# Kernel optimization log

Hardware: AMD Instinct MI355X
Metric: run time of the kernel (lower is better)

Reference implementation:

```python
import jax, jax.numpy as jnp
import numpy as np

TOTAL = 16777216  # total nodes across all graphs
N = 65536         # number of graphs (len(v_count))
K = 16            # k_pool


def setup_inputs() -> dict:
    key = jax.random.key(0)
    k1, k2 = jax.random.split(key)
    Y = jax.random.normal(k1, (TOTAL, 1), dtype=jnp.float32)
    W = jnp.ones((K,), dtype=jnp.float32)  # initializer Ones, as in build()
    e_map = jnp.sort(jax.random.randint(k2, (TOTAL,), 0, N, dtype=jnp.int32))
    v_count = jnp.ones((N,), dtype=jnp.int32)  # only its length is used
    return {"Y": Y, "W": W, "e_map": e_map, "v_count": v_count}


def reference(Y, W, e_map, v_count):
    # Faithful SortPooling forward. Instead of materializing the padded
    # [N, max_seg_len] -inf tensor, we do k_pool fused segment-max passes:
    # each pass extracts the current per-segment max and masks out exactly
    # one occurrence (the first, by index) -- identical to tf.math.top_k on
    # the -inf-padded ragged-to-dense tensor (ties yield duplicate values,
    # matching top_k semantics).
    n = v_count.shape[0]
    k = W.shape[0]  # static k_pool; segments here are much larger than k
    y = jnp.squeeze(Y, axis=-1)  # [TOTAL]
    total = y.shape[0]
    idxs = jnp.arange(total, dtype=jnp.int32)
    neg_inf = jnp.float32(-jnp.inf)

    y_work = y
    tops = []
    for _ in range(k):
        m = jax.ops.segment_max(y_work, e_map, num_segments=n)  # [N]
        tops.append(m)
        is_max = y_work == m[e_map]
        # first index attaining the max in each segment (total == sentinel)
        first = jax.ops.segment_min(jnp.where(is_max, idxs, total),
                                    e_map, num_segments=n)  # [N]
        # OOB indices (exhausted/empty segments) are dropped by scatter
        y_work = y_work.at[first].set(neg_inf)

    Y_top = jnp.stack(tops, axis=-1)        # [N, k] sorted descending
    Wn = jax.nn.softmax(W)                  # [k]
    Y_w = jnp.where(jnp.isinf(Y_top), jnp.float32(0.0), Y_top) * Wn
    return jnp.sum(Y_w, axis=-1)            # [N]
```

## Files before the change

### kernel.cpp

```cpp
#include <hip/hip_runtime.h>
#include <math.h>

#define KPOOL 16
#define SPLIT 8

typedef float f32x4 __attribute__((ext_vector_type(4)));

__device__ __forceinline__ void ce(float& x, float& y) {
  float hi = fmaxf(x, y), lo = fminf(x, y);
  x = hi;
  y = lo;
}

__device__ __forceinline__ void sort8(float (&v)[8]) {
  ce(v[0], v[1]); ce(v[2], v[3]); ce(v[4], v[5]); ce(v[6], v[7]);
  ce(v[0], v[2]); ce(v[1], v[3]); ce(v[4], v[6]); ce(v[5], v[7]);
  ce(v[1], v[2]); ce(v[5], v[6]);
  ce(v[0], v[4]); ce(v[1], v[5]); ce(v[2], v[6]); ce(v[3], v[7]);
  ce(v[2], v[4]); ce(v[3], v[5]);
  ce(v[1], v[2]); ce(v[3], v[4]); ce(v[5], v[6]);
}

__device__ __forceinline__ void merge8into16(float (&t)[KPOOL], const float (&b)[8]) {
#pragma unroll
  for (int i = 8; i < 16; ++i) t[i] = fmaxf(t[i], b[15 - i]);
#pragma unroll
  for (int s = 8; s >= 1; s >>= 1) {
#pragma unroll
    for (int i = 0; i < 16; ++i)
      if ((i & s) == 0) ce(t[i], t[i + s]);
  }
}

__device__ __forceinline__ void merge_partner(float (&t)[KPOOL], int dist) {
  float c[KPOOL];
#pragma unroll
  for (int i = 0; i < KPOOL; ++i) {
    float o = __shfl_xor(t[KPOOL - 1 - i], dist);
    c[i] = fmaxf(t[i], o);
  }
#pragma unroll
  for (int s = 8; s >= 1; s >>= 1) {
#pragma unroll
    for (int i = 0; i < KPOOL; ++i)
      if ((i & s) == 0) ce(c[i], c[i + s]);
  }
#pragma unroll
  for (int i = 0; i < KPOOL; ++i) t[i] = c[i];
}

__device__ __forceinline__ int lower_bound_range(const int* __restrict__ a,
                                                 int lo, int hi, int key) {
  while (lo < hi) {
    int mid = (lo + hi) >> 1;
    if (a[mid] < key) lo = mid + 1;
    else hi = mid;
  }
  return lo;
}

__global__ __launch_bounds__(256)
void boundary_kernel(const int* __restrict__ emap, int total, int n,
                     int* __restrict__ starts, float* __restrict__ wn_out,
                     const float* __restrict__ W) {
  int g = blockIdx.x * 256 + threadIdx.x;
  if (g == 0) {
    float w[KPOOL], m = -INFINITY, s = 0.0f;
#pragma unroll
    for (int k = 0; k < KPOOL; ++k) { w[k] = W[k]; m = fmaxf(m, w[k]); }
#pragma unroll
    for (int k = 0; k < KPOOL; ++k) { w[k] = expf(w[k] - m); s += w[k]; }
#pragma unroll
    for (int k = 0; k < KPOOL; ++k) wn_out[k] = w[k] / s;
  }
  if (g > n) return;
  long long E = (long long)g * total / n;
  int wlo = (int)(E - 8192 > 0 ? E - 8192 : 0);
  int whi = (int)(E + 8192 < total ? E + 8192 : total);
  bool ok = ((wlo == 0) || (emap[wlo - 1] < g)) &&
            ((whi == total) || (emap[whi] >= g));
  if (!ok) { wlo = 0; whi = total; }
  starts[g] = lower_bound_range(emap, wlo, whi, g);
}

__global__ __launch_bounds__(256, 8)
void sortpool_main(const float* __restrict__ Y, const float* __restrict__ W,
                   const int* __restrict__ starts, const float* __restrict__ Wn,
                   const int* __restrict__ emap,
                   float* __restrict__ out, int total, int n) {
  const int tid = blockIdx.x * 256 + threadIdx.x;
  const int g = tid >> 3;
  const int q = tid & 7;
  if (g >= n) return;

  int s0, s1;
  if (starts) {
    s0 = starts[g];
    s1 = starts[g + 1];
  } else {
    s0 = lower_bound_range(emap, 0, total, g);
    s1 = lower_bound_range(emap, 0, total, g + 1);
  }
  const unsigned len = (unsigned)(s1 - s0);

  const int B0 = s0 >> 3;
  const int B1 = (s1 + 7) >> 3;

  float t[KPOOL];
#pragma unroll
  for (int i = 0; i < KPOOL; ++i) t[i] = -INFINITY;

  int b = B0 + q;
  f32x4 c0 = 0, c1 = 0;
  if (b < B1) {
    const f32x4* p = reinterpret_cast<const f32x4*>(Y + (b << 3));
    c0 = p[0];
    c1 = p[1];
  }
#pragma unroll 1
  while (b < B1) {
    const int bn = b + SPLIT;
    f32x4 n0 = 0, n1 = 0;
    if (bn < B1) {
      const f32x4* p = reinterpret_cast<const f32x4*>(Y + (bn << 3));
      n0 = p[0];
      n1 = p[1];
    }
    const int base = b << 3;
    float v[8] = {c0[0], c0[1], c0[2], c0[3], c1[0], c1[1], c1[2], c1[3]};
#pragma unroll
    for (int j = 0; j < 8; ++j) {
      if ((unsigned)(base + j - s0) >= len) v[j] = -INFINITY;
    }
    sort8(v);
    merge8into16(t, v);
    c0 = n0;
    c1 = n1;
    b = bn;
  }

  merge_partner(t, 1);
  merge_partner(t, 2);
  merge_partner(t, 4);

  float res = 0.0f;
  if (Wn) {
#pragma unroll
    for (int k = 0; k < KPOOL; ++k) {
      float tv = t[k];
      res += (tv > -INFINITY) ? tv * Wn[k] : 0.0f;
    }
  } else {
    float wv[KPOOL], m = -INFINITY, s = 0.0f;
#pragma unroll
    for (int k = 0; k < KPOOL; ++k) { wv[k] = W[k]; m = fmaxf(m, wv[k]); }
#pragma unroll
    for (int k = 0; k < KPOOL; ++k) { wv[k] = expf(wv[k] - m); s += wv[k]; }
    const float inv = 1.0f / s;
#pragma unroll
    for (int k = 0; k < KPOOL; ++k) {
      float tv = t[k];
      res += (tv > -INFINITY) ? tv * (wv[k] * inv) : 0.0f;
    }
  }

  if (q == 0) out[g] = res;
}

extern "C" void kernel_launch(void* const* d_in, const int* in_sizes, int n_in,
                              void* d_out, int out_size, void* d_ws, size_t ws_size,
                              hipStream_t stream) {
  const float* Y = (const float*)d_in[0];
  const float* W = (const float*)d_in[1];
  const int* emap = (const int*)d_in[2];
  const int total = in_sizes[0];
  const int n = in_sizes[3];
  float* out = (float*)d_out;

  int* starts = (int*)d_ws;
  float* wn_buf = (float*)((char*)d_ws + (size_t)(n + 1) * sizeof(int));
  const bool use_ws =
      (ws_size >= (size_t)(n + 1) * sizeof(int) + KPOOL * sizeof(float));

  if (use_ws) {
    int nb = (n + 1 + 255) / 256;
    boundary_kernel<<<nb, 256, 0, stream>>>(emap, total, n, starts, wn_buf, W);
  }

  long long threads = (long long)n * SPLIT;
  int blocks = (int)((threads + 255) / 256);
  sortpool_main<<<blocks, 256, 0, stream>>>(Y, W, use_ws ? starts : nullptr,
                                            use_ws ? wn_buf : nullptr,
                                            emap, out, total, n);
}
```

Before: 37.11 us.

## Fuse boundary search and softmax into main kernel with interpolation search

Removes the separate boundary kernel and workspace. Each wavefront now computes its nine segment boundaries in-kernel using an interpolation guess followed by a narrow binary search, then shares them across lanes with shuffles. The softmax weights are computed per wave through shuffle reductions. The main loop also processes two 8-element blocks per iteration with 4-wide prefetch, which adds register pressure (launch bounds lowered to 6) to cut one launch and the dependent round trip through global memory.

```diff
diff --git a/kernel.cpp b/kernel.cpp
--- a/kernel.cpp
+++ b/kernel.cpp
@@ -49,8 +49,8 @@
   for (int i = 0; i < KPOOL; ++i) t[i] = c[i];
 }
 
-__device__ __forceinline__ int lower_bound_range(const int* __restrict__ a,
-                                                 int lo, int hi, int key) {
+__device__ __forceinline__ int lb_range(const int* __restrict__ a, int lo,
+                                        int hi, int key) {
   while (lo < hi) {
     int mid = (lo + hi) >> 1;
     if (a[mid] < key) lo = mid + 1;
@@ -59,83 +59,100 @@
   return lo;
 }
 
-__global__ __launch_bounds__(256)
-void boundary_kernel(const int* __restrict__ emap, int total, int n,
-                     int* __restrict__ starts, float* __restrict__ wn_out,
-                     const float* __restrict__ W) {
-  int g = blockIdx.x * 256 + threadIdx.x;
-  if (g == 0) {
-    float w[KPOOL], m = -INFINITY, s = 0.0f;
-#pragma unroll
-    for (int k = 0; k < KPOOL; ++k) { w[k] = W[k]; m = fmaxf(m, w[k]); }
-#pragma unroll
-    for (int k = 0; k < KPOOL; ++k) { w[k] = expf(w[k] - m); s += w[k]; }
-#pragma unroll
-    for (int k = 0; k < KPOOL; ++k) wn_out[k] = w[k] / s;
-  }
-  if (g > n) return;
-  long long E = (long long)g * total / n;
-  int wlo = (int)(E - 8192 > 0 ? E - 8192 : 0);
-  int whi = (int)(E + 8192 < total ? E + 8192 : total);
-  bool ok = ((wlo == 0) || (emap[wlo - 1] < g)) &&
-            ((whi == total) || (emap[whi] >= g));
-  if (!ok) { wlo = 0; whi = total; }
-  starts[g] = lower_bound_range(emap, wlo, whi, g);
+__device__ __forceinline__ int lb_interp(const int* __restrict__ a, int total,
+                                         int n, int key) {
+  if (key <= 0) return 0;
+  if (key >= n) return total;
+  long long E = (long long)key * total / n;
+  if (E > total - 1) E = total - 1;
+  int v0 = a[(int)E];
+  long long p1 = E + (long long)(key - v0) * total / n;
+  int lo = (int)(p1 - 512 < 0 ? 0 : p1 - 512);
+  int hi = (int)(p1 + 512 > total ? (long long)total : p1 + 512);
+  bool ok = (lo == 0 || a[lo - 1] < key) && (hi == total || a[hi] >= key);
+  if (!ok) { lo = 0; hi = total; }
+  return lb_range(a, lo, hi, key);
 }
 
-__global__ __launch_bounds__(256, 8)
-void sortpool_main(const float* __restrict__ Y, const float* __restrict__ W,
-                   const int* __restrict__ starts, const float* __restrict__ Wn,
-                   const int* __restrict__ emap,
-                   float* __restrict__ out, int total, int n) {
+__global__ __launch_bounds__(256, 6)
+void sortpool_fused(const float* __restrict__ Y, const float* __restrict__ W,
+                    const int* __restrict__ emap, float* __restrict__ out,
+                    int total, int n) {
   const int tid = blockIdx.x * 256 + threadIdx.x;
+  const int lane = threadIdx.x & 63;
   const int g = tid >> 3;
   const int q = tid & 7;
-  if (g >= n) return;
+  const int gj = lane >> 3;
+  const int g0 = (tid >> 6) << 3;
+  const bool valid = (g < n);
 
-  int s0, s1;
-  if (starts) {
-    s0 = starts[g];
-    s1 = starts[g + 1];
-  } else {
-    s0 = lower_bound_range(emap, 0, total, g);
-    s1 = lower_bound_range(emap, 0, total, g + 1);
+  int bd = 0;
+  {
+    int key = g0 + lane;
+    if (lane < 9 && key <= n) bd = lb_interp(emap, total, n, key);
   }
+  int s0 = __shfl(bd, gj);
+  int s1 = __shfl(bd, gj + 1);
+  if (!valid) { s0 = 0; s1 = 0; }
+
+  float wn_l;
+  {
+    float w = (lane < KPOOL) ? W[lane] : -INFINITY;
+    float m = w;
+#pragma unroll
+    for (int d = 1; d < KPOOL; d <<= 1) m = fmaxf(m, __shfl_xor(m, d));
+    float e = (lane < KPOOL) ? expf(w - m) : 0.0f;
+    float s = e;
+#pragma unroll
+    for (int d = 1; d < KPOOL; d <<= 1) s += __shfl_xor(s, d);
+    wn_l = e / s;
+  }
+
   const unsigned len = (unsigned)(s1 - s0);
-
   const int B0 = s0 >> 3;
   const int B1 = (s1 + 7) >> 3;
+  const int BMAX = (total >> 3) - 1;
 
   float t[KPOOL];
 #pragma unroll
   for (int i = 0; i < KPOOL; ++i) t[i] = -INFINITY;
 
-  int b = B0 + q;
-  f32x4 c0 = 0, c1 = 0;
+  int b = B0 + 2 * q;
+  f32x4 c0 = 0, c1 = 0, c2 = 0, c3 = 0;
   if (b < B1) {
-    const f32x4* p = reinterpret_cast<const f32x4*>(Y + (b << 3));
-    c0 = p[0];
-    c1 = p[1];
+    const f32x4* pA = reinterpret_cast<const f32x4*>(Y + (b << 3));
+    int bB = b + 1 < BMAX ? b + 1 : BMAX;
+    const f32x4* pB = reinterpret_cast<const f32x4*>(Y + (bB << 3));
+    c0 = pA[0]; c1 = pA[1]; c2 = pB[0]; c3 = pB[1];
   }
 #pragma unroll 1
   while (b < B1) {
-    const int bn = b + SPLIT;
-    f32x4 n0 = 0, n1 = 0;
+    const int bn = b + 2 * SPLIT;
+    f32x4 p0 = 0, p1 = 0, p2 = 0, p3 = 0;
     if (bn < B1) {
-      const f32x4* p = reinterpret_cast<const f32x4*>(Y + (bn << 3));
-      n0 = p[0];
-      n1 = p[1];
+      const f32x4* pA = reinterpret_cast<const f32x4*>(Y + (bn << 3));
+      int bB = bn + 1 < BMAX ? bn + 1 : BMAX;
+      const f32x4* pB = reinterpret_cast<const f32x4*>(Y + (bB << 3));
+      p0 = pA[0]; p1 = pA[1]; p2 = pB[0]; p3 = pB[1];
     }
     const int base = b << 3;
-    float v[8] = {c0[0], c0[1], c0[2], c0[3], c1[0], c1[1], c1[2], c1[3]};
+    {
+      float v[8] = {c0[0], c0[1], c0[2], c0[3], c1[0], c1[1], c1[2], c1[3]};
 #pragma unroll
-    for (int j = 0; j < 8; ++j) {
-      if ((unsigned)(base + j - s0) >= len) v[j] = -INFINITY;
+      for (int jj = 0; jj < 8; ++jj)
+        if ((unsigned)(base + jj - s0) >= len) v[jj] = -INFINITY;
+      sort8(v);
+      merge8into16(t, v);
     }
-    sort8(v);
-    merge8into16(t, v);
-    c0 = n0;
-    c1 = n1;
+    {
+      float u[8] = {c2[0], c2[1], c2[2], c2[3], c3[0], c3[1], c3[2], c3[3]};
+#pragma unroll
+      for (int jj = 0; jj < 8; ++jj)
+        if ((unsigned)(base + 8 + jj - s0) >= len) u[jj] = -INFINITY;
+      sort8(u);
+      merge8into16(t, u);
+    }
+    c0 = p0; c1 = p1; c2 = p2; c3 = p3;
     b = bn;
   }
 
@@ -144,27 +161,14 @@
   merge_partner(t, 4);
 
   float res = 0.0f;
-  if (Wn) {
 #pragma unroll
-    for (int k = 0; k < KPOOL; ++k) {
-      float tv = t[k];
-      res += (tv > -INFINITY) ? tv * Wn[k] : 0.0f;
-    }
-  } else {
-    float wv[KPOOL], m = -INFINITY, s = 0.0f;
-#pragma unroll
-    for (int k = 0; k < KPOOL; ++k) { wv[k] = W[k]; m = fmaxf(m, wv[k]); }
-#pragma unroll
-    for (int k = 0; k < KPOOL; ++k) { wv[k] = expf(wv[k] - m); s += wv[k]; }
-    const float inv = 1.0f / s;
-#pragma unroll
-    for (int k = 0; k < KPOOL; ++k) {
-      float tv = t[k];
-      res += (tv > -INFINITY) ? tv * (wv[k] * inv) : 0.0f;
-    }
+  for (int k = 0; k < KPOOL; ++k) {
+    float wk = __shfl(wn_l, k);
+    float tv = t[k];
+    res += (tv > -INFINITY) ? tv * wk : 0.0f;
   }
 
-  if (q == 0) out[g] = res;
+  if (valid && q == 0) out[g] = res;
 }
 
 extern "C" void kernel_launch(void* const* d_in, const int* in_sizes, int n_in,
@@ -177,19 +181,7 @@
   const int n = in_sizes[3];
   float* out = (float*)d_out;
 
-  int* starts = (int*)d_ws;
-  float* wn_buf = (float*)((char*)d_ws + (size_t)(n + 1) * sizeof(int));
-  const bool use_ws =
-      (ws_size >= (size_t)(n + 1) * sizeof(int) + KPOOL * sizeof(float));
-
-  if (use_ws) {
-    int nb = (n + 1 + 255) / 256;
-    boundary_kernel<<<nb, 256, 0, stream>>>(emap, total, n, starts, wn_buf, W);
-  }
-
   long long threads = (long long)n * SPLIT;
   int blocks = (int)((threads + 255) / 256);
-  sortpool_main<<<blocks, 256, 0, stream>>>(Y, W, use_ws ? starts : nullptr,
-                                            use_ws ? wn_buf : nullptr,
-                                            emap, out, total, n);
+  sortpool_fused<<<blocks, 256, 0, stream>>>(Y, W, emap, out, total, n);
 }
```

Result: slower. 38.08 us (+2.6%).

## Use 8-way parallel search for segment starts and unpredicated prefetch in main loop

Applied to the files above, without the earlier changes.

The boundary kernel replaces its windowed binary search with an 8-ary search over a fixed 32768-element window. It probes 7 pivots per level so the independent loads can be in flight together, cutting the chain of dependent memory accesses. The main kernel now prefetches unconditionally using clamped addresses, which removes branches around the loads. Launch bounds drop from 8 to 4 blocks per CU, and the workspace/no-workspace paths are split into separate kernels. The risks are lower occupancy and some redundant loads at segment tails.

```diff
diff --git a/kernel.cpp b/kernel.cpp
--- a/kernel.cpp
+++ b/kernel.cpp
@@ -49,8 +49,8 @@
   for (int i = 0; i < KPOOL; ++i) t[i] = c[i];
 }
 
-__device__ __forceinline__ int lower_bound_range(const int* __restrict__ a,
-                                                 int lo, int hi, int key) {
+__device__ __forceinline__ int lb_range(const int* __restrict__ a, int lo,
+                                        int hi, int key) {
   while (lo < hi) {
     int mid = (lo + hi) >> 1;
     if (a[mid] < key) lo = mid + 1;
@@ -63,7 +63,7 @@
 void boundary_kernel(const int* __restrict__ emap, int total, int n,
                      int* __restrict__ starts, float* __restrict__ wn_out,
                      const float* __restrict__ W) {
-  int g = blockIdx.x * 256 + threadIdx.x;
+  const int g = blockIdx.x * 256 + threadIdx.x;
   if (g == 0) {
     float w[KPOOL], m = -INFINITY, s = 0.0f;
 #pragma unroll
@@ -74,96 +74,158 @@
     for (int k = 0; k < KPOOL; ++k) wn_out[k] = w[k] / s;
   }
   if (g > n) return;
-  long long E = (long long)g * total / n;
-  int wlo = (int)(E - 8192 > 0 ? E - 8192 : 0);
-  int whi = (int)(E + 8192 < total ? E + 8192 : total);
-  bool ok = ((wlo == 0) || (emap[wlo - 1] < g)) &&
-            ((whi == total) || (emap[whi] >= g));
-  if (!ok) { wlo = 0; whi = total; }
-  starts[g] = lower_bound_range(emap, wlo, whi, g);
-}
-
-__global__ __launch_bounds__(256, 8)
-void sortpool_main(const float* __restrict__ Y, const float* __restrict__ W,
-                   const int* __restrict__ starts, const float* __restrict__ Wn,
-                   const int* __restrict__ emap,
+  if (g == 0) { starts[0] = 0; return; }
+  if (g >= n) { starts[n] = total; return; }
+
+  const int key = g;
+  const int W0 = 32768;
+  if (total < W0) { starts[g] = lb_range(emap, 0, total, key); return; }
+
+  long long E = (long long)key * total / n;
+  int wlo = (int)(E - W0 / 2);
+  if (wlo < 0) wlo = 0;
+  if (wlo > total - W0) wlo = total - W0;
+
+  int p[7];
+#pragma unroll
+  for (int k = 0; k < 7; ++k) p[k] = emap[wlo + (k + 1) * 4096];
+  const int vlo = (wlo > 0) ? emap[wlo - 1] : (key - 1) - key;
+  const int vhi = emap[wlo + W0 - 1];
+  const bool ok = (vlo < key) && ((wlo + W0 == total) || (vhi >= key));
+  if (!ok) { starts[g] = lb_range(emap, 0, total, key); return; }
+
+  int lo = wlo;
+  int c = 0;
+#pragma unroll
+  for (int k = 0; k < 7; ++k) c += (p[k] < key) ? 1 : 0;
+  lo += c * 4096;
+
+#pragma unroll
+  for (int w8 = 512; w8 >= 1; w8 >>= 3) {
+#pragma unroll
+    for (int k = 0; k < 7; ++k) p[k] = emap[lo + (k + 1) * w8];
+    c = 0;
+#pragma unroll
+    for (int k = 0; k < 7; ++k) c += (p[k] < key) ? 1 : 0;
+    lo += c * w8;
+  }
+  starts[g] = (emap[lo] < key) ? lo + 1 : lo;
+}
+
+__global__ __launch_bounds__(256, 4)
+void sortpool_main(const float* __restrict__ Y,
+                   const int* __restrict__ starts,
+                   const float* __restrict__ Wn,
                    float* __restrict__ out, int total, int n) {
   const int tid = blockIdx.x * 256 + threadIdx.x;
   const int g = tid >> 3;
   const int q = tid & 7;
   if (g >= n) return;
 
-  int s0, s1;
-  if (starts) {
-    s0 = starts[g];
-    s1 = starts[g + 1];
-  } else {
-    s0 = lower_bound_range(emap, 0, total, g);
-    s1 = lower_bound_range(emap, 0, total, g + 1);
-  }
+  const int s0 = starts[g];
+  const int s1 = starts[g + 1];
   const unsigned len = (unsigned)(s1 - s0);
 
   const int B0 = s0 >> 3;
   const int B1 = (s1 + 7) >> 3;
+  const int BLAST = (total >> 3) - 1;
 
   float t[KPOOL];
 #pragma unroll
   for (int i = 0; i < KPOOL; ++i) t[i] = -INFINITY;
 
   int b = B0 + q;
-  f32x4 c0 = 0, c1 = 0;
-  if (b < B1) {
-    const f32x4* p = reinterpret_cast<const f32x4*>(Y + (b << 3));
-    c0 = p[0];
-    c1 = p[1];
-  }
+  {
+    const int a0 = b <= BLAST ? b : BLAST;
+    const f32x4* p = reinterpret_cast<const f32x4*>(Y + (a0 << 3));
+    f32x4 c0 = p[0];
+    f32x4 c1 = p[1];
+#pragma unroll 1
+    while (b < B1) {
+      const int bn = b + SPLIT;
+      const int an = bn < B1 ? bn : b;
+      const f32x4* pn = reinterpret_cast<const f32x4*>(Y + (an << 3));
+      f32x4 n0 = pn[0];
+      f32x4 n1 = pn[1];
+      const int base = b << 3;
+      float v[8] = {c0[0], c0[1], c0[2], c0[3], c1[0], c1[1], c1[2], c1[3]};
+#pragma unroll
+      for (int jj = 0; jj < 8; ++jj) {
+        if ((unsigned)(base + jj - s0) >= len) v[jj] = -INFINITY;
+      }
+      sort8(v);
+      merge8into16(t, v);
+      c0 = n0;
+      c1 = n1;
+      b = bn;
+    }
+  }
+
+  merge_partner(t, 1);
+  merge_partner(t, 2);
+  merge_partner(t, 4);
+
+  float res = 0.0f;
+#pragma unroll
+  for (int k = 0; k < KPOOL; ++k) {
+    float tv = t[k];
+    res += (tv > -INFINITY) ? tv * Wn[k] : 0.0f;
+  }
+
+  if (q == 0) out[g] = res;
+}
+
+__global__ __launch_bounds__(256, 4)
+void sortpool_main_nows(const float* __restrict__ Y, const float* __restrict__ W,
+                        const int* __restrict__ emap, float* __restrict__ out,
+                        int total, int n) {
+  const int tid = blockIdx.x * 256 + threadIdx.x;
+  const int g = tid >> 3;
+  const int q = tid & 7;
+  if (g >= n) return;
+  const int s0 = lb_range(emap, 0, total, g);
+  const int s1 = lb_range(emap, 0, total, g + 1);
+  const unsigned len = (unsigned)(s1 - s0);
+  const int B0 = s0 >> 3;
+  const int B1 = (s1 + 7) >> 3;
+  const int BLAST = (total >> 3) - 1;
+  float t[KPOOL];
+#pragma unroll
+  for (int i = 0; i < KPOOL; ++i) t[i] = -INFINITY;
+  int b = B0 + q;
+  const int a0 = b <= BLAST ? b : BLAST;
+  const f32x4* p = reinterpret_cast<const f32x4*>(Y + (a0 << 3));
+  f32x4 c0 = p[0], c1 = p[1];
 #pragma unroll 1
   while (b < B1) {
     const int bn = b + SPLIT;
-    f32x4 n0 = 0, n1 = 0;
-    if (bn < B1) {
-      const f32x4* p = reinterpret_cast<const f32x4*>(Y + (bn << 3));
-      n0 = p[0];
-      n1 = p[1];
-    }
+    const int an = bn < B1 ? bn : b;
+    const f32x4* pn = reinterpret_cast<const f32x4*>(Y + (an << 3));
+    f32x4 n0 = pn[0], n1 = pn[1];
     const int base = b << 3;
     float v[8] = {c0[0], c0[1], c0[2], c0[3], c1[0], c1[1], c1[2], c1[3]};
 #pragma unroll
-    for (int j = 0; j < 8; ++j) {
-      if ((unsigned)(base + j - s0) >= len) v[j] = -INFINITY;
-    }
+    for (int jj = 0; jj < 8; ++jj)
+      if ((unsigned)(base + jj - s0) >= len) v[jj] = -INFINITY;
     sort8(v);
     merge8into16(t, v);
-    c0 = n0;
-    c1 = n1;
-    b = bn;
-  }
-
+    c0 = n0; c1 = n1; b = bn;
+  }
   merge_partner(t, 1);
   merge_partner(t, 2);
   merge_partner(t, 4);
-
+  float wv[KPOOL], m = -INFINITY, s = 0.0f;
+#pragma unroll
+  for (int k = 0; k < KPOOL; ++k) { wv[k] = W[k]; m = fmaxf(m, wv[k]); }
+#pragma unroll
+  for (int k = 0; k < KPOOL; ++k) { wv[k] = expf(wv[k] - m); s += wv[k]; }
+  const float inv = 1.0f / s;
   float res = 0.0f;
-  if (Wn) {
-#pragma unroll
-    for (int k = 0; k < KPOOL; ++k) {
-      float tv = t[k];
-      res += (tv > -INFINITY) ? tv * Wn[k] : 0.0f;
-    }
-  } else {
-    float wv[KPOOL], m = -INFINITY, s = 0.0f;
-#pragma unroll
-    for (int k = 0; k < KPOOL; ++k) { wv[k] = W[k]; m = fmaxf(m, wv[k]); }
-#pragma unroll
-    for (int k = 0; k < KPOOL; ++k) { wv[k] = expf(wv[k] - m); s += wv[k]; }
-    const float inv = 1.0f / s;
-#pragma unroll
-    for (int k = 0; k < KPOOL; ++k) {
-      float tv = t[k];
-      res += (tv > -INFINITY) ? tv * (wv[k] * inv) : 0.0f;
-    }
-  }
-
+#pragma unroll
+  for (int k = 0; k < KPOOL; ++k) {
+    float tv = t[k];
+    res += (tv > -INFINITY) ? tv * (wv[k] * inv) : 0.0f;
+  }
   if (q == 0) out[g] = res;
 }
 
@@ -182,14 +244,14 @@
   const bool use_ws =
       (ws_size >= (size_t)(n + 1) * sizeof(int) + KPOOL * sizeof(float));
 
+  long long threads = (long long)n * SPLIT;
+  int blocks = (int)((threads + 255) / 256);
+
   if (use_ws) {
     int nb = (n + 1 + 255) / 256;
     boundary_kernel<<<nb, 256, 0, stream>>>(emap, total, n, starts, wn_buf, W);
-  }
-
-  long long threads = (long long)n * SPLIT;
-  int blocks = (int)((threads + 255) / 256);
-  sortpool_main<<<blocks, 256, 0, stream>>>(Y, W, use_ws ? starts : nullptr,
-                                            use_ws ? wn_buf : nullptr,
-                                            emap, out, total, n);
-}
+    sortpool_main<<<blocks, 256, 0, stream>>>(Y, starts, wn_buf, out, total, n);
+  } else {
+    sortpool_main_nows<<<blocks, 256, 0, stream>>>(Y, W, emap, out, total, n);
+  }
+}
```

Result: no change. 37.50 us (+1.1%).
